# Optimization experiments

Hardware: AMD Instinct MI355X
Metric: run time of the kernel (lower is better)

The kernel has to match this reference:

```python
import jax, jax.numpy as jnp
import numpy as np
from jax import lax

H = 512; MEL = 80; B = 8; S = 128; T = 200; NCH = 256


def _lstm_layer(x, Wih, Whh, bih, bhh, reverse=False):
    # x: [B, S, Din] -> [B, S, H]; PyTorch gate order i,f,g,o
    xs = jnp.swapaxes(x, 0, 1)
    bsz = x.shape[0]
    hid = Whh.shape[1]

    def step(carry, xt):
        h, c = carry
        g = xt @ Wih.T + bih + h @ Whh.T + bhh
        i, f, gg, o = jnp.split(g, 4, axis=-1)
        c2 = jax.nn.sigmoid(f) * c + jax.nn.sigmoid(i) * jnp.tanh(gg)
        h2 = jax.nn.sigmoid(o) * jnp.tanh(c2)
        return (h2, c2), h2

    init = (jnp.zeros((bsz, hid), x.dtype), jnp.zeros((bsz, hid), x.dtype))
    _, hs = lax.scan(step, init, xs, reverse=reverse)
    return jnp.swapaxes(hs, 0, 1)


def _forward(text_sequence, target_mel_len, emb, Wih00, Whh00, bih00, bhh00,
             Wih01, Whh01, bih01, bhh01, Wih10, Whh10, bih10, bhh10,
             Wih11, Whh11, bih11, bhh11, attn_W, attn_b, attn_v,
             dec_Wih, dec_Whh, dec_bih, dec_bhh, mel_W, mel_b):
    x = emb[text_sequence]  # [B,S,H] (dropout disabled: eval mode)
    f0 = _lstm_layer(x, Wih00, Whh00, bih00, bhh00)
    b0 = _lstm_layer(x, Wih01, Whh01, bih01, bhh01, reverse=True)
    x1 = jnp.concatenate([f0, b0], axis=-1)
    f1 = _lstm_layer(x1, Wih10, Whh10, bih10, bhh10)
    b1 = _lstm_layer(x1, Wih11, Whh11, bih11, bhh11, reverse=True)
    enc = jnp.concatenate([f1, b1], axis=-1)  # [B,S,2H]

    # attn Linear on cat(hidden, encoder): split weight into hidden/encoder parts
    W_h = attn_W[:, :H]
    W_e = attn_W[:, H:]
    enc_part = jnp.einsum('bsd,hd->bsh', enc, W_e) + attn_b  # hoisted out of loop
    bsz = text_sequence.shape[0]

    def step(carry, _):
        h, c, din = carry
        energy = jnp.tanh(enc_part + (h @ W_h.T)[:, None, :])  # [B,S,H]
        score = energy @ attn_v                                # [B,S]
        a = jax.nn.softmax(score, axis=1)
        ctx = jnp.einsum('bs,bsd->bd', a, enc)                 # [B,2H]
        xin = jnp.concatenate([din, ctx], axis=1)              # [B,MEL+2H]
        g = xin @ dec_Wih.T + dec_bih + h @ dec_Whh.T + dec_bhh
        i, f, gg, o = jnp.split(g, 4, axis=-1)
        c2 = jax.nn.sigmoid(f) * c + jax.nn.sigmoid(i) * jnp.tanh(gg)
        h2 = jax.nn.sigmoid(o) * jnp.tanh(c2)
        mel = h2 @ mel_W.T + mel_b                             # [B,MEL]
        return (h2, c2, mel), mel

    carry0 = (jnp.zeros((bsz, H), jnp.float32),
              jnp.zeros((bsz, H), jnp.float32),
              jnp.zeros((bsz, MEL), jnp.float32))
    _, mels = lax.scan(step, carry0, None, length=target_mel_len)
    return jnp.transpose(mels, (1, 2, 0))  # [B, MEL, T]


def setup_inputs() -> dict:
    key = jax.random.key(0)
    keys = jax.random.split(key, 64)
    ki = iter(range(64))

    def rn(shape, scale=0.05):
        return jax.random.normal(keys[next(ki)], shape, dtype=jnp.float32) * scale

    inp = {}
    inp['text_sequence'] = jax.random.randint(keys[next(ki)], (B, S), 0, NCH)
    inp['target_mel_len'] = T
    inp['emb'] = rn((NCH, H), 0.3)
    for l, din in ((0, H), (1, 2 * H)):
        for d in (0, 1):
            inp[f'Wih{l}{d}'] = rn((4 * H, din))
            inp[f'Whh{l}{d}'] = rn((4 * H, H))
            inp[f'bih{l}{d}'] = rn((4 * H,))
            inp[f'bhh{l}{d}'] = rn((4 * H,))
    inp['attn_W'] = rn((H, 3 * H))
    inp['attn_b'] = rn((H,))
    inp['attn_v'] = rn((H,))
    inp['dec_Wih'] = rn((4 * H, 2 * H + MEL))
    inp['dec_Whh'] = rn((4 * H, H))
    inp['dec_bih'] = rn((4 * H,))
    inp['dec_bhh'] = rn((4 * H,))
    inp['mel_W'] = rn((MEL, H))
    inp['mel_b'] = rn((MEL,))
    return inp


def reference(text_sequence, target_mel_len, emb, Wih00, Whh00, bih00, bhh00,
              Wih01, Whh01, bih01, bhh01, Wih10, Whh10, bih10, bhh10,
              Wih11, Whh11, bih11, bhh11, attn_W, attn_b, attn_v,
              dec_Wih, dec_Whh, dec_bih, dec_bhh, mel_W, mel_b):
    return _forward(text_sequence, target_mel_len, emb, Wih00, Whh00, bih00, bhh00,
                    Wih01, Whh01, bih01, bhh01, Wih10, Whh10, bih10, bhh10,
                    Wih11, Whh11, bih11, bhh11, attn_W, attn_b, attn_v,
                    dec_Wih, dec_Whh, dec_bih, dec_bhh, mel_W, mel_b)
```

## Files before the change

kernel.cpp:

```cpp
#include <hip/hip_runtime.h>

#define B_ 8
#define S_ 128
#define H_ 512
#define G_ 2048
#define MEL_ 80

#define FLG_DEC    0
#define FLG_L0     8192
#define FLG_L1     10240
#define OFF_H0S    12288
#define OFF_H1S    28672
#define OFF_DH     45056
#define OFF_ATT    53248
#define OFF_HW     54272
#define ZERO_WORDS 58368
#define OFF_X0     58368
#define OFF_GX0F   (OFF_X0 + 524288)
#define OFF_GX0B   (OFF_GX0F + 2097152)
#define OFF_H0     (OFF_GX0B + 2097152)
#define OFF_GX1F   (OFF_H0 + 1048576)
#define OFF_GX1B   (OFF_GX1F + 2097152)
#define OFF_ENC    (OFF_GX1B + 2097152)
#define OFF_ENCP   (OFF_ENC + 1048576)
#define OFF_WE     OFF_GX0F
#define OFF_WH2    OFF_GX0B
#define OFF_BA     (OFF_GX0B + 1048576)
#define OFF_BB     (OFF_GX0B + 1050624)

__device__ __forceinline__ float sigm_f(float x) {
    x = fminf(fmaxf(x, -30.f), 30.f);
    return 1.f / (1.f + __expf(-x));
}
__device__ __forceinline__ float tanh_f(float x) {
    x = fminf(fmaxf(x, -15.f), 15.f);
    float e = __expf(2.f * x);
    return (e - 1.f) / (e + 1.f);
}

__device__ __forceinline__ void agw_u(unsigned* p, unsigned v) {
    __hip_atomic_store(p, v, __ATOMIC_RELAXED, __HIP_MEMORY_SCOPE_AGENT);
}
__device__ __forceinline__ unsigned agr_u(const unsigned* p) {
    return __hip_atomic_load(p, __ATOMIC_RELAXED, __HIP_MEMORY_SCOPE_AGENT);
}
__device__ __forceinline__ void agw_f(float* p, float v) {
    agw_u((unsigned*)p, __float_as_uint(v));
}

__device__ __forceinline__ float4 agr_f4(const float* p) {
    float4 v;
    asm volatile("global_load_dwordx4 %0, %1, off sc1\n\t"
                 "s_waitcnt vmcnt(0)"
                 : "=v"(v) : "v"(p) : "memory");
    return v;
}

__global__ __launch_bounds__(256) void zero_kernel(float* p) {
    p[blockIdx.x * 256 + threadIdx.x] = 0.f;
}

__global__ __launch_bounds__(256) void embed_kernel(const int* __restrict__ text,
                                                    const float* __restrict__ emb,
                                                    float* __restrict__ X) {
    int i = blockIdx.x * 256 + threadIdx.x;
    int bs = i >> 7;
    int h4 = i & 127;
    int ch = text[bs];
    ((float4*)X)[i] = ((const float4*)emb)[ch * 128 + h4];
}

__global__ __launch_bounds__(256) void gemm_f32(const float* __restrict__ A, int lda,
                                                const float* __restrict__ W, int ldw,
                                                const float* __restrict__ b1,
                                                const float* __restrict__ b2,
                                                float* __restrict__ C, int ldc, int K) {
    __shared__ float As[32][68];
    __shared__ float Ws[32][68];
    int tid = threadIdx.x;
    int tx = tid & 15, ty = tid >> 4;
    int n0 = blockIdx.x * 64, m0 = blockIdx.y * 64;
    float acc[4][4] = {};
    int r  = tid >> 3;
    int c4 = (tid & 7) * 4;
    for (int k0 = 0; k0 < K; k0 += 32) {
        float4 a0 = *(const float4*)&A[(m0 + r) * lda + k0 + c4];
        float4 a1 = *(const float4*)&A[(m0 + r + 32) * lda + k0 + c4];
        float4 w0 = *(const float4*)&W[(n0 + r) * ldw + k0 + c4];
        float4 w1 = *(const float4*)&W[(n0 + r + 32) * ldw + k0 + c4];
        As[c4 + 0][r] = a0.x; As[c4 + 1][r] = a0.y; As[c4 + 2][r] = a0.z; As[c4 + 3][r] = a0.w;
        As[c4 + 0][r + 32] = a1.x; As[c4 + 1][r + 32] = a1.y; As[c4 + 2][r + 32] = a1.z; As[c4 + 3][r + 32] = a1.w;
        Ws[c4 + 0][r] = w0.x; Ws[c4 + 1][r] = w0.y; Ws[c4 + 2][r] = w0.z; Ws[c4 + 3][r] = w0.w;
        Ws[c4 + 0][r + 32] = w1.x; Ws[c4 + 1][r + 32] = w1.y; Ws[c4 + 2][r + 32] = w1.z; Ws[c4 + 3][r + 32] = w1.w;
        __syncthreads();
#pragma unroll 8
        for (int kk = 0; kk < 32; ++kk) {
            float4 av = *(const float4*)&As[kk][ty * 4];
            float4 wv = *(const float4*)&Ws[kk][tx * 4];
            acc[0][0] = fmaf(av.x, wv.x, acc[0][0]); acc[0][1] = fmaf(av.x, wv.y, acc[0][1]);
            acc[0][2] = fmaf(av.x, wv.z, acc[0][2]); acc[0][3] = fmaf(av.x, wv.w, acc[0][3]);
            acc[1][0] = fmaf(av.y, wv.x, acc[1][0]); acc[1][1] = fmaf(av.y, wv.y, acc[1][1]);
            acc[1][2] = fmaf(av.y, wv.z, acc[1][2]); acc[1][3] = fmaf(av.y, wv.w, acc[1][3]);
            acc[2][0] = fmaf(av.z, wv.x, acc[2][0]); acc[2][1] = fmaf(av.z, wv.y, acc[2][1]);
            acc[2][2] = fmaf(av.z, wv.z, acc[2][2]); acc[2][3] = fmaf(av.z, wv.w, acc[2][3]);
            acc[3][0] = fmaf(av.w, wv.x, acc[3][0]); acc[3][1] = fmaf(av.w, wv.y, acc[3][1]);
            acc[3][2] = fmaf(av.w, wv.z, acc[3][2]); acc[3][3] = fmaf(av.w, wv.w, acc[3][3]);
        }
        __syncthreads();
    }
#pragma unroll
    for (int i = 0; i < 4; ++i)
#pragma unroll
        for (int j = 0; j < 4; ++j) {
            int n = n0 + tx * 4 + j;
            int m = m0 + ty * 4 + i;
            float bias = (b1 ? b1[n] : 0.f) + (b2 ? b2[n] : 0.f);
            C[m * ldc + n] = acc[i][j] + bias;
        }
}

__global__ __launch_bounds__(256) void we_kernel(const float* __restrict__ Wih,
                                                 const float* __restrict__ ENC,
                                                 float* __restrict__ WE) {
    const float* A = Wih + 80;
    const float* W = ENC + (size_t)blockIdx.z * 131072;
    float* C = WE + (size_t)blockIdx.z * 262144;
    __shared__ float As[32][68];
    __shared__ float Ws[32][68];
    int tid = threadIdx.x;
    int tx = tid & 15, ty = tid >> 4;
    int n0 = blockIdx.x * 64, m0 = blockIdx.y * 64;
    float acc[4][4] = {};
    int r  = tid >> 3;
    int c4 = (tid & 7) * 4;
    for (int k0 = 0; k0 < 1024; k0 += 32) {
        float4 a0 = *(const float4*)&A[(size_t)(m0 + r) * 1104 + k0 + c4];
        float4 a1 = *(const float4*)&A[(size_t)(m0 + r + 32) * 1104 + k0 + c4];
        float4 w0 = *(const float4*)&W[(n0 + r) * 1024 + k0 + c4];
        float4 w1 = *(const float4*)&W[(n0 + r + 32) * 1024 + k0 + c4];
        As[c4 + 0][r] = a0.x; As[c4 + 1][r] = a0.y; As[c4 + 2][r] = a0.z; As[c4 + 3][r] = a0.w;
        As[c4 + 0][r + 32] = a1.x; As[c4 + 1][r + 32] = a1.y; As[c4 + 2][r + 32] = a1.z; As[c4 + 3][r + 32] = a1.w;
        Ws[c4 + 0][r] = w0.x; Ws[c4 + 1][r] = w0.y; Ws[c4 + 2][r] = w0.z; Ws[c4 + 3][r] = w0.w;
        Ws[c4 + 0][r + 32] = w1.x; Ws[c4 + 1][r + 32] = w1.y; Ws[c4 + 2][r + 32] = w1.z; Ws[c4 + 3][r + 32] = w1.w;
        __syncthreads();
#pragma unroll 8
        for (int kk = 0; kk < 32; ++kk) {
            float4 av = *(const float4*)&As[kk][ty * 4];
            float4 wv = *(const float4*)&Ws[kk][tx * 4];
            acc[0][0] = fmaf(av.x, wv.x, acc[0][0]); acc[0][1] = fmaf(av.x, wv.y, acc[0][1]);
            acc[0][2] = fmaf(av.x, wv.z, acc[0][2]); acc[0][3] = fmaf(av.x, wv.w, acc[0][3]);
            acc[1][0] = fmaf(av.y, wv.x, acc[1][0]); acc[1][1] = fmaf(av.y, wv.y, acc[1][1]);
            acc[1][2] = fmaf(av.y, wv.z, acc[1][2]); acc[1][3] = fmaf(av.y, wv.w, acc[1][3]);
            acc[2][0] = fmaf(av.z, wv.x, acc[2][0]); acc[2][1] = fmaf(av.z, wv.y, acc[2][1]);
            acc[2][2] = fmaf(av.z, wv.z, acc[2][2]); acc[2][3] = fmaf(av.z, wv.w, acc[2][3]);
            acc[3][0] = fmaf(av.w, wv.x, acc[3][0]); acc[3][1] = fmaf(av.w, wv.y, acc[3][1]);
            acc[3][2] = fmaf(av.w, wv.z, acc[3][2]); acc[3][3] = fmaf(av.w, wv.w, acc[3][3]);
        }
        __syncthreads();
    }
#pragma unroll
    for (int i = 0; i < 4; ++i)
#pragma unroll
        for (int j = 0; j < 4; ++j)
            C[(size_t)(m0 + ty * 4 + i) * 128 + n0 + tx * 4 + j] = acc[i][j];
}

__global__ __launch_bounds__(256) void wh2_kernel(const float* __restrict__ Wih,
                                                  const float* __restrict__ Whh,
                                                  const float* __restrict__ melW,
                                                  float* __restrict__ WH2) {
    int wg = blockIdx.x;
    int tid = threadIdx.x;
    int r = wg >> 1;
    int k = (wg & 1) * 256 + tid;
    __shared__ float wrow[80];
    if (tid < 80) wrow[tid] = Wih[(size_t)r * 1104 + tid];
    __syncthreads();
    float acc = Whh[(size_t)r * 512 + k];
#pragma unroll 8
    for (int m = 0; m < 80; ++m)
        acc = fmaf(wrow[m], melW[m * 512 + k], acc);
    WH2[(size_t)r * 512 + k] = acc;
}

__global__ __launch_bounds__(256) void bias_kernel(const float* __restrict__ Wih,
                                                   const float* __restrict__ bih,
                                                   const float* __restrict__ bhh,
                                                   const float* __restrict__ melb,
                                                   float* __restrict__ BA,
                                                   float* __restrict__ BB) {
    int r = blockIdx.x * 256 + threadIdx.x;
    float a = bih[r] + bhh[r];
    float b2 = 0.f;
#pragma unroll 8
    for (int m = 0; m < 80; ++m)
        b2 = fmaf(Wih[(size_t)r * 1104 + m], melb[m], b2);
    BA[r] = a;
    BB[r] = a + b2;
}

__global__ __launch_bounds__(256) void lstm_kernel(const float* __restrict__ GXf,
                                                   const float* __restrict__ GXb,
                                                   const float* __restrict__ Whh_f,
                                                   const float* __restrict__ Whh_b,
                                                   float* __restrict__ Hout,
                                                   float* __restrict__ hstate,
                                                   unsigned* __restrict__ flagsL) {
    int wg  = blockIdx.x;
    int s   = wg & 7;
    int g16 = wg >> 3;
    int dir = g16 >> 3;
    int b   = g16 & 7;
    const float* GX  = dir ? GXb : GXf;
    const float* Whh = dir ? Whh_b : Whh_f;
    float* hs = hstate + g16 * 1024;
    unsigned* fg = flagsL + g16 * 128;

    int tid = threadIdx.x;
    int g = tid >> 6, c = tid & 63;
    int grow = g * 512 + s * 64 + c;
    const float* wr = Whh + (size_t)grow * 512;

    __shared__ float hsh[512];
    __shared__ float gvL[4][64];

    float cst = 0.f;

    for (int t = 0; t < 128; ++t) {
        if (tid < 128) {
            const unsigned* f = fg + (tid >> 4) * 16;
            while (agr_u(f) < (unsigned)t)
                __builtin_amdgcn_s_sleep(1);
            *(float4*)&hsh[tid * 4] = agr_f4(hs + (t & 1) * 512 + tid * 4);
        }
        __syncthreads();

        int st = dir ? (127 - t) : t;
        float acc = GX[((size_t)b * S_ + st) * G_ + grow];
        float a0 = 0.f, a1 = 0.f, a2 = 0.f, a3 = 0.f;
#pragma unroll 8
        for (int k = 0; k < 512; k += 4) {
            float4 wv = *(const float4*)(wr + k);
            float4 hv = *(const float4*)&hsh[k];
            a0 = fmaf(wv.x, hv.x, a0); a1 = fmaf(wv.y, hv.y, a1);
            a2 = fmaf(wv.z, hv.z, a2); a3 = fmaf(wv.w, hv.w, a3);
        }
        gvL[g][c] = acc + (a0 + a1) + (a2 + a3);
        __syncthreads();

        if (tid < 64) {
            float gi = gvL[0][tid], gf = gvL[1][tid];
            float gg = gvL[2][tid], go = gvL[3][tid];
            float c2 = sigm_f(gf) * cst + sigm_f(gi) * tanh_f(gg);
            float h2 = sigm_f(go) * tanh_f(c2);
            cst = c2;
            agw_f(hs + ((t & 1) ^ 1) * 512 + s * 64 + tid, h2);
            asm volatile("s_waitcnt vmcnt(0)" ::: "memory");
            if (tid == 0)
                agw_u(fg + s * 16, (unsigned)(t + 1));
            Hout[((size_t)b * S_ + st) * 1024 + dir * 512 + s * 64 + tid] = h2;
        }
    }
}

__global__ __launch_bounds__(256) void decoder_kernel(float* __restrict__ ws,
                                                      const float* __restrict__ attn_W,
                                                      const float* __restrict__ attn_v,
                                                      const float* __restrict__ mel_W,
                                                      const float* __restrict__ mel_b,
                                                      float* __restrict__ out, int T,
                                                      unsigned* __restrict__ flags) {
    float* ENCP = ws + OFF_ENCP;
    float* DH   = ws + OFF_DH;
    float* ATT  = ws + OFF_ATT;
    float* HW   = ws + OFF_HW;
    const float* WE  = ws + OFF_WE;
    const float* WH2 = ws + OFF_WH2;
    const float* BA  = ws + OFF_BA;
    const float* BB  = ws + OFF_BB;

    int wg  = blockIdx.x;
    int tid = threadIdx.x;

    if (wg < 128) {
        int s = wg & 15;
        int b = wg >> 4;
        unsigned* fC = flags + b * 1024;
        unsigned* fA = fC + 16 * 16;
        unsigned* fB = fC + 32 * 16;

        int r   = tid >> 1;
        int half = tid & 1;
        int grow = (r >> 5) * 512 + s * 32 + (r & 31);
        const float* wh2_half = WH2 + (size_t)grow * 512 + half * 256;
        const float* we_row   = WE + ((size_t)b * 2048 + grow) * 128 + half * 64;
        float bias_a = (half == 0) ? BA[grow] : 0.f;
        float bias_b = (half == 0) ? BB[grow] : 0.f;
        int r2 = tid & 31, oct = tid >> 5;
        const float* wh_row = attn_W + (size_t)(s * 32 + r2) * 1536 + oct * 64;

        __shared__ float hsh[512];
        __shared__ float hwred[32][9];
        __shared__ float gBx[128][2];
        __shared__ float gv[128];
        __shared__ float attL[128];

        float cst = 0.f;

        for (int t = 0; t < T; ++t) {
            if (tid < 128) {
                const unsigned* f = fC + (tid >> 3) * 16;
                while (agr_u(f) < (unsigned)t)
                    __builtin_amdgcn_s_sleep(1);
                *(float4*)&hsh[tid * 4] = agr_f4(DH + (t & 1) * 4096 + b * 512 + tid * 4);
            }
            __syncthreads();

            {
                const float* hp = hsh + oct * 64;
                float w = 0.f;
#pragma unroll 8
                for (int k = 0; k < 64; k += 4) {
                    float4 wv = *(const float4*)(wh_row + k);
                    float4 hv = *(const float4*)(hp + k);
                    w = fmaf(wv.x, hv.x, w); w = fmaf(wv.y, hv.y, w);
                    w = fmaf(wv.z, hv.z, w); w = fmaf(wv.w, hv.w, w);
                }
                hwred[r2][oct] = w;
            }
            __syncthreads();
            if (tid < 32) {
                float hw = hwred[tid][0] + hwred[tid][1] + hwred[tid][2] + hwred[tid][3]
                         + hwred[tid][4] + hwred[tid][5] + hwred[tid][6] + hwred[tid][7];
                agw_f(HW + b * 512 + s * 32 + tid, hw);
                asm volatile("s_waitcnt vmcnt(0)" ::: "memory");
                if (tid == 0)
                    agw_u(fA + s * 16, (unsigned)(t + 1));
            }

            float wpart = (t == 0) ? bias_a : bias_b;
            {
                const float* hp = hsh + half * 256;
                float a0 = 0.f, a1 = 0.f, a2 = 0.f, a3 = 0.f;
#pragma unroll 8
                for (int k = 0; k < 256; k += 4) {
                    float4 wv = *(const float4*)(wh2_half + k);
                    float4 hv = *(const float4*)(hp + k);
                    a0 = fmaf(wv.x, hv.x, a0); a1 = fmaf(wv.y, hv.y, a1);
                    a2 = fmaf(wv.z, hv.z, a2); a3 = fmaf(wv.w, hv.w, a3);
                }
                wpart += (a0 + a1) + (a2 + a3);
            }

            if (tid < 32) {
                while (agr_u(fB) < (unsigned)(t + 1))
                    __builtin_amdgcn_s_sleep(1);
                *(float4*)&attL[tid * 4] = agr_f4(ATT + b * 128 + tid * 4);
            }
            __syncthreads();

            {
                const float* ap = attL + half * 64;
                float a0 = 0.f, a1 = 0.f, a2 = 0.f, a3 = 0.f;
#pragma unroll 8
                for (int k = 0; k < 64; k += 4) {
                    float4 wv = *(const float4*)(we_row + k);
                    a0 = fmaf(wv.x, ap[k + 0], a0); a1 = fmaf(wv.y, ap[k + 1], a1);
                    a2 = fmaf(wv.z, ap[k + 2], a2); a3 = fmaf(wv.w, ap[k + 3], a3);
                }
                gBx[r][half] = wpart + (a0 + a1) + (a2 + a3);
            }
            __syncthreads();
            if (tid < 128)
                gv[tid] = gBx[tid][0] + gBx[tid][1];
            __syncthreads();
            if (tid < 32) {
                float gi = gv[tid], gf = gv[32 + tid], gg = gv[64 + tid], go = gv[96 + tid];
                float c2 = sigm_f(gf) * cst + sigm_f(gi) * tanh_f(gg);
                float h2 = sigm_f(go) * tanh_f(c2);
                cst = c2;
                agw_f(DH + ((t + 1) & 1) * 4096 + b * 512 + s * 32 + tid, h2);
                asm volatile("s_waitcnt vmcnt(0)" ::: "memory");
                if (tid == 0)
                    agw_u(fC + s * 16, (unsigned)(t + 1));
            }
        }
    } else {
        int b = wg - 128;
        unsigned* fC = flags + b * 1024;
        unsigned* fA = fC + 16 * 16;
        unsigned* fB = fC + 32 * 16;

        __shared__ float hw2[512];
        __shared__ float dh2[512];
        __shared__ float scred[128][2];
        __shared__ float red[128];
        __shared__ float att[128];
        __shared__ float melp[80][2];

        int r = tid >> 1, half = tid & 1;

        for (int t = 0; t < T; ++t) {
            if (tid < 128) {
                const unsigned* f = fA + (tid >> 3) * 16;
                while (agr_u(f) < (unsigned)(t + 1))
                    __builtin_amdgcn_s_sleep(1);
                *(float4*)&hw2[tid * 4] = agr_f4(HW + b * 512 + tid * 4);
            }
            __syncthreads();

            {
                int sI = tid & 127, kh = tid >> 7;
                const float* ep = ENCP + ((size_t)b * S_ + sI) * 512 + kh * 256;
                const float* hp = hw2 + kh * 256;
                const float* vv = attn_v + kh * 256;
                float a0 = 0.f, a1 = 0.f, a2 = 0.f, a3 = 0.f;
#pragma unroll 4
                for (int k = 0; k < 256; k += 4) {
                    float4 e4 = *(const float4*)(ep + k);
                    float4 h4 = *(const float4*)(hp + k);
                    float4 v4 = *(const float4*)(vv + k);
                    a0 = fmaf(tanh_f(e4.x + h4.x), v4.x, a0);
                    a1 = fmaf(tanh_f(e4.y + h4.y), v4.y, a1);
                    a2 = fmaf(tanh_f(e4.z + h4.z), v4.z, a2);
                    a3 = fmaf(tanh_f(e4.w + h4.w), v4.w, a3);
                }
                scred[sI][kh] = (a0 + a1) + (a2 + a3);
            }
            __syncthreads();

            float sc = 0.f;
            if (tid < 128) {
                sc = scred[tid][0] + scred[tid][1];
                red[tid] = sc;
            }
            __syncthreads();
            for (int off = 64; off >= 1; off >>= 1) {
                if (tid < off) red[tid] = fmaxf(red[tid], red[tid + off]);
                __syncthreads();
            }
            float mx = red[0];
            __syncthreads();
            if (tid < 128) {
                float e = __expf(sc - mx);
                att[tid] = e;
                red[tid] = e;
            }
            __syncthreads();
            if (tid < 64) red[tid] += red[tid + 64];
            __syncthreads();
            for (int off = 32; off >= 1; off >>= 1) {
                if (tid < off) red[tid] += red[tid + off];
                __syncthreads();
            }
            float inv = 1.f / red[0];

            if (tid < 32) {
                agw_f(ATT + b * 128 + tid * 4 + 0, att[tid * 4 + 0] * inv);
                agw_f(ATT + b * 128 + tid * 4 + 1, att[tid * 4 + 1] * inv);
                agw_f(ATT + b * 128 + tid * 4 + 2, att[tid * 4 + 2] * inv);
                agw_f(ATT + b * 128 + tid * 4 + 3, att[tid * 4 + 3] * inv);
                asm volatile("s_waitcnt vmcnt(0)" ::: "memory");
                if (tid == 0)
                    agw_u(fB, (unsigned)(t + 1));
            }

            if (t > 0) {
                if (tid < 128) {
                    const unsigned* f = fC + (tid >> 3) * 16;
                    while (agr_u(f) < (unsigned)t)
                        __builtin_amdgcn_s_sleep(1);
                    *(float4*)&dh2[tid * 4] = agr_f4(DH + (t & 1) * 4096 + b * 512 + tid * 4);
                }
                __syncthreads();
                if (tid < 160) {
                    const float* wp = mel_W + (size_t)r * 512 + half * 256;
                    const float* hp = dh2 + half * 256;
                    float a0 = 0.f, a1 = 0.f, a2 = 0.f, a3 = 0.f;
#pragma unroll 8
                    for (int k = 0; k < 256; k += 4) {
                        float4 wv = *(const float4*)(wp + k);
                        float4 hv = *(const float4*)(hp + k);
                        a0 = fmaf(wv.x, hv.x, a0); a1 = fmaf(wv.y, hv.y, a1);
                        a2 = fmaf(wv.z, hv.z, a2); a3 = fmaf(wv.w, hv.w, a3);
                    }
                    melp[r][half] = (a0 + a1) + (a2 + a3);
                }
                __syncthreads();
                if (tid < 80)
                    out[b * MEL_ * T + tid * T + (t - 1)] = melp[tid][0] + melp[tid][1] + mel_b[tid];
            }
        }

        if (tid < 128) {
            const unsigned* f = fC + (tid >> 3) * 16;
            while (agr_u(f) < (unsigned)T)
                __builtin_amdgcn_s_sleep(1);
            *(float4*)&dh2[tid * 4] = agr_f4(DH + (T & 1) * 4096 + b * 512 + tid * 4);
        }
        __syncthreads();
        if (tid < 160) {
            const float* wp = mel_W + (size_t)r * 512 + half * 256;
            const float* hp = dh2 + half * 256;
            float a0 = 0.f, a1 = 0.f, a2 = 0.f, a3 = 0.f;
#pragma unroll 8
            for (int k = 0; k < 256; k += 4) {
                float4 wv = *(const float4*)(wp + k);
                float4 hv = *(const float4*)(hp + k);
                a0 = fmaf(wv.x, hv.x, a0); a1 = fmaf(wv.y, hv.y, a1);
                a2 = fmaf(wv.z, hv.z, a2); a3 = fmaf(wv.w, hv.w, a3);
            }
            melp[r][half] = (a0 + a1) + (a2 + a3);
        }
        __syncthreads();
        if (tid < 80)
            out[b * MEL_ * T + tid * T + (T - 1)] = melp[tid][0] + melp[tid][1] + mel_b[tid];
    }
}

extern "C" void kernel_launch(void* const* d_in, const int* in_sizes, int n_in,
                              void* d_out, int out_size, void* d_ws, size_t ws_size,
                              hipStream_t stream) {
    const int*   text  = (const int*)d_in[0];
    const float* emb   = (const float*)d_in[2];
    const float* Wih00 = (const float*)d_in[3];
    const float* Whh00 = (const float*)d_in[4];
    const float* bih00 = (const float*)d_in[5];
    const float* bhh00 = (const float*)d_in[6];
    const float* Wih01 = (const float*)d_in[7];
    const float* Whh01 = (const float*)d_in[8];
    const float* bih01 = (const float*)d_in[9];
    const float* bhh01 = (const float*)d_in[10];
    const float* Wih10 = (const float*)d_in[11];
    const float* Whh10 = (const float*)d_in[12];
    const float* bih10 = (const float*)d_in[13];
    const float* bhh10 = (const float*)d_in[14];
    const float* Wih11 = (const float*)d_in[15];
    const float* Whh11 = (const float*)d_in[16];
    const float* bih11 = (const float*)d_in[17];
    const float* bhh11 = (const float*)d_in[18];
    const float* attn_W = (const float*)d_in[19];
    const float* attn_b = (const float*)d_in[20];
    const float* attn_v = (const float*)d_in[21];
    const float* dec_Wih = (const float*)d_in[22];
    const float* dec_Whh = (const float*)d_in[23];
    const float* dec_bih = (const float*)d_in[24];
    const float* dec_bhh = (const float*)d_in[25];
    const float* mel_W = (const float*)d_in[26];
    const float* mel_b = (const float*)d_in[27];

    float* ws = (float*)d_ws;
    unsigned* flags = (unsigned*)d_ws;
    float* out = (float*)d_out;
    int T = out_size / (B_ * MEL_);

    zero_kernel<<<ZERO_WORDS / 256, 256, 0, stream>>>(ws);

    embed_kernel<<<512, 256, 0, stream>>>(text, emb, ws + OFF_X0);

    gemm_f32<<<dim3(32, 16), 256, 0, stream>>>(ws + OFF_X0, 512, Wih00, 512,
                                               bih00, bhh00, ws + OFF_GX0F, 2048, 512);
    gemm_f32<<<dim3(32, 16), 256, 0, stream>>>(ws + OFF_X0, 512, Wih01, 512,
                                               bih01, bhh01, ws + OFF_GX0B, 2048, 512);
    lstm_kernel<<<128, 256, 0, stream>>>(ws + OFF_GX0F, ws + OFF_GX0B, Whh00, Whh01,
                                         ws + OFF_H0, ws + OFF_H0S, flags + FLG_L0);
    wh2_kernel<<<4096, 256, 0, stream>>>(dec_Wih, dec_Whh, mel_W, ws + OFF_WH2);
    bias_kernel<<<8, 256, 0, stream>>>(dec_Wih, dec_bih, dec_bhh, mel_b,
                                       ws + OFF_BA, ws + OFF_BB);
    gemm_f32<<<dim3(32, 16), 256, 0, stream>>>(ws + OFF_H0, 1024, Wih10, 1024,
                                               bih10, bhh10, ws + OFF_GX1F, 2048, 1024);
    gemm_f32<<<dim3(32, 16), 256, 0, stream>>>(ws + OFF_H0, 1024, Wih11, 1024,
                                               bih11, bhh11, ws + OFF_GX1B, 2048, 1024);
    lstm_kernel<<<128, 256, 0, stream>>>(ws + OFF_GX1F, ws + OFF_GX1B, Whh10, Whh11,
                                         ws + OFF_ENC, ws + OFF_H1S, flags + FLG_L1);
    gemm_f32<<<dim3(8, 16), 256, 0, stream>>>(ws + OFF_ENC, 1024, attn_W + 512, 1536,
                                              attn_b, nullptr, ws + OFF_ENCP, 512, 1024);
    we_kernel<<<dim3(2, 32, 8), 256, 0, stream>>>(dec_Wih, ws + OFF_ENC, ws + OFF_WE);
    decoder_kernel<<<136, 256, 0, stream>>>(ws, attn_W, attn_v, mel_W, mel_b, out, T,
                                            flags + FLG_DEC);
}
```

Baseline: 9.927 ms.

## Compute attention hidden projection as partial sums after cell update to shorten critical path

The h·W_h attention projection is no longer computed at the start of each decoder step by the cell workgroups. Instead, each cell workgroup multiplies its freshly computed 32-element slice of h2 against the matching columns of attn_W and publishes 512-wide partial sums. The attention workgroup waits on a new per-slice flag and reduces the 16 partials itself. This takes the projection off the step's serial critical path and removes one cross-workgroup handshake, at the cost of more global traffic for the partial sums plus an extra zeroing launch.

Result: no change. 9.902 ms (-0.3%).

```diff
diff --git a/kernel.cpp b/kernel.cpp
--- a/kernel.cpp
+++ b/kernel.cpp
@@ -27,6 +27,7 @@
 #define OFF_WH2    OFF_GX0B
 #define OFF_BA     (OFF_GX0B + 1048576)
 #define OFF_BB     (OFF_GX0B + 1050624)
+#define OFF_HWP    OFF_GX1F
 
 __device__ __forceinline__ float sigm_f(float x) {
     x = fminf(fmaxf(x, -30.f), 30.f);
@@ -54,6 +55,21 @@
                  "s_waitcnt vmcnt(0)"
                  : "=v"(v) : "v"(p) : "memory");
     return v;
+}
+__device__ __forceinline__ void agw_f4(float* p, float4 v) {
+    agw_f(p + 0, v.x); agw_f(p + 1, v.y); agw_f(p + 2, v.z); agw_f(p + 3, v.w);
+    asm volatile("s_waitcnt vmcnt(0)" ::: "memory");
+}
+__device__ __forceinline__ void agr_f4x4(const float* p0, const float* p1,
+                                         const float* p2, const float* p3,
+                                         float4& a, float4& b, float4& c, float4& d) {
+    asm volatile("global_load_dwordx4 %0, %4, off sc1\n\t"
+                 "global_load_dwordx4 %1, %5, off sc1\n\t"
+                 "global_load_dwordx4 %2, %6, off sc1\n\t"
+                 "global_load_dwordx4 %3, %7, off sc1\n\t"
+                 "s_waitcnt vmcnt(0)"
+                 : "=&v"(a), "=&v"(b), "=&v"(c), "=&v"(d)
+                 : "v"(p0), "v"(p1), "v"(p2), "v"(p3) : "memory");
 }
 
 __global__ __launch_bounds__(256) void zero_kernel(float* p) {
@@ -273,7 +289,7 @@
     float* ENCP = ws + OFF_ENCP;
     float* DH   = ws + OFF_DH;
     float* ATT  = ws + OFF_ATT;
-    float* HW   = ws + OFF_HW;
+    float* HWP  = ws + OFF_HWP;
     const float* WE  = ws + OFF_WE;
     const float* WH2 = ws + OFF_WH2;
     const float* BA  = ws + OFF_BA;
@@ -285,9 +301,9 @@
     if (wg < 128) {
         int s = wg & 15;
         int b = wg >> 4;
-        unsigned* fC = flags + b * 1024;
-        unsigned* fA = fC + 16 * 16;
-        unsigned* fB = fC + 32 * 16;
+        unsigned* fCh = flags + b * 1024;
+        unsigned* fCp = fCh + 256;
+        unsigned* fB  = fCh + 512;
 
         int r   = tid >> 1;
         int half = tid & 1;
@@ -296,47 +312,23 @@
         const float* we_row   = WE + ((size_t)b * 2048 + grow) * 128 + half * 64;
         float bias_a = (half == 0) ? BA[grow] : 0.f;
         float bias_b = (half == 0) ? BB[grow] : 0.f;
-        int r2 = tid & 31, oct = tid >> 5;
-        const float* wh_row = attn_W + (size_t)(s * 32 + r2) * 1536 + oct * 64;
 
         __shared__ float hsh[512];
-        __shared__ float hwred[32][9];
         __shared__ float gBx[128][2];
         __shared__ float gv[128];
         __shared__ float attL[128];
+        __shared__ float h2sh[32];
 
         float cst = 0.f;
 
         for (int t = 0; t < T; ++t) {
             if (tid < 128) {
-                const unsigned* f = fC + (tid >> 3) * 16;
+                const unsigned* f = fCh + (tid >> 3) * 16;
                 while (agr_u(f) < (unsigned)t)
                     __builtin_amdgcn_s_sleep(1);
                 *(float4*)&hsh[tid * 4] = agr_f4(DH + (t & 1) * 4096 + b * 512 + tid * 4);
             }
             __syncthreads();
-
-            {
-                const float* hp = hsh + oct * 64;
-                float w = 0.f;
-#pragma unroll 8
-                for (int k = 0; k < 64; k += 4) {
-                    float4 wv = *(const float4*)(wh_row + k);
-                    float4 hv = *(const float4*)(hp + k);
-                    w = fmaf(wv.x, hv.x, w); w = fmaf(wv.y, hv.y, w);
-                    w = fmaf(wv.z, hv.z, w); w = fmaf(wv.w, hv.w, w);
-                }
-                hwred[r2][oct] = w;
-            }
-            __syncthreads();
-            if (tid < 32) {
-                float hw = hwred[tid][0] + hwred[tid][1] + hwred[tid][2] + hwred[tid][3]
-                         + hwred[tid][4] + hwred[tid][5] + hwred[tid][6] + hwred[tid][7];
-                agw_f(HW + b * 512 + s * 32 + tid, hw);
-                asm volatile("s_waitcnt vmcnt(0)" ::: "memory");
-                if (tid == 0)
-                    agw_u(fA + s * 16, (unsigned)(t + 1));
-            }
 
             float wpart = (t == 0) ? bias_a : bias_b;
             {
@@ -374,23 +366,49 @@
             if (tid < 128)
                 gv[tid] = gBx[tid][0] + gBx[tid][1];
             __syncthreads();
+
             if (tid < 32) {
                 float gi = gv[tid], gf = gv[32 + tid], gg = gv[64 + tid], go = gv[96 + tid];
                 float c2 = sigm_f(gf) * cst + sigm_f(gi) * tanh_f(gg);
                 float h2 = sigm_f(go) * tanh_f(c2);
                 cst = c2;
+                h2sh[tid] = h2;
                 agw_f(DH + ((t + 1) & 1) * 4096 + b * 512 + s * 32 + tid, h2);
                 asm volatile("s_waitcnt vmcnt(0)" ::: "memory");
                 if (tid == 0)
-                    agw_u(fC + s * 16, (unsigned)(t + 1));
-            }
+                    agw_u(fCh + s * 16, (unsigned)(t + 1));
+            }
+            __syncthreads();
+
+            if (tid < 128) {
+                int r0 = tid * 4;
+                float p[4];
+#pragma unroll
+                for (int i = 0; i < 4; ++i) {
+                    const float* wrow2 = attn_W + (size_t)(r0 + i) * 1536 + s * 32;
+                    float a0 = 0.f, a1 = 0.f, a2 = 0.f, a3 = 0.f;
+#pragma unroll
+                    for (int c = 0; c < 32; c += 4) {
+                        float4 wv = *(const float4*)(wrow2 + c);
+                        a0 = fmaf(wv.x, h2sh[c + 0], a0); a1 = fmaf(wv.y, h2sh[c + 1], a1);
+                        a2 = fmaf(wv.z, h2sh[c + 2], a2); a3 = fmaf(wv.w, h2sh[c + 3], a3);
+                    }
+                    p[i] = (a0 + a1) + (a2 + a3);
+                }
+                float4 v; v.x = p[0]; v.y = p[1]; v.z = p[2]; v.w = p[3];
+                agw_f4(HWP + ((size_t)(b * 16 + s)) * 512 + r0, v);
+            }
+            __syncthreads();
+            if (tid == 0)
+                agw_u(fCp + s * 16, (unsigned)(t + 1));
         }
     } else {
         int b = wg - 128;
-        unsigned* fC = flags + b * 1024;
-        unsigned* fA = fC + 16 * 16;
-        unsigned* fB = fC + 32 * 16;
-
+        unsigned* fCh = flags + b * 1024;
+        unsigned* fCp = fCh + 256;
+        unsigned* fB  = fCh + 512;
+
+        __shared__ float hwp2[2][512];
         __shared__ float hw2[512];
         __shared__ float dh2[512];
         __shared__ float scred[128][2];
@@ -401,11 +419,33 @@
         int r = tid >> 1, half = tid & 1;
 
         for (int t = 0; t < T; ++t) {
+            if (tid < 16) {
+                while (agr_u(fCp + tid * 16) < (unsigned)t)
+                    __builtin_amdgcn_s_sleep(1);
+            }
+            __syncthreads();
+
+            {
+                int c4 = (tid & 127), jh = tid >> 7;
+                const float* base = HWP + (size_t)b * 8192 + (size_t)jh * 8 * 512 + c4 * 4;
+                float4 v0, v1, v2, v3, v4, v5, v6, v7;
+                agr_f4x4(base + 0 * 512, base + 1 * 512, base + 2 * 512, base + 3 * 512,
+                         v0, v1, v2, v3);
+                agr_f4x4(base + 4 * 512, base + 5 * 512, base + 6 * 512, base + 7 * 512,
+                         v4, v5, v6, v7);
+                float4 sum;
+                sum.x = ((v0.x + v1.x) + (v2.x + v3.x)) + ((v4.x + v5.x) + (v6.x + v7.x));
+                sum.y = ((v0.y + v1.y) + (v2.y + v3.y)) + ((v4.y + v5.y) + (v6.y + v7.y));
+                sum.z = ((v0.z + v1.z) + (v2.z + v3.z)) + ((v4.z + v5.z) + (v6.z + v7.z));
+                sum.w = ((v0.w + v1.w) + (v2.w + v3.w)) + ((v4.w + v5.w) + (v6.w + v7.w));
+                *(float4*)&hwp2[jh][c4 * 4] = sum;
+            }
+            __syncthreads();
             if (tid < 128) {
-                const unsigned* f = fA + (tid >> 3) * 16;
-                while (agr_u(f) < (unsigned)(t + 1))
-                    __builtin_amdgcn_s_sleep(1);
-                *(float4*)&hw2[tid * 4] = agr_f4(HW + b * 512 + tid * 4);
+                float4 a = *(const float4*)&hwp2[0][tid * 4];
+                float4 c = *(const float4*)&hwp2[1][tid * 4];
+                float4 s4; s4.x = a.x + c.x; s4.y = a.y + c.y; s4.z = a.z + c.z; s4.w = a.w + c.w;
+                *(float4*)&hw2[tid * 4] = s4;
             }
             __syncthreads();
 
@@ -466,12 +506,8 @@
             }
 
             if (t > 0) {
-                if (tid < 128) {
-                    const unsigned* f = fC + (tid >> 3) * 16;
-                    while (agr_u(f) < (unsigned)t)
-                        __builtin_amdgcn_s_sleep(1);
+                if (tid < 128)
                     *(float4*)&dh2[tid * 4] = agr_f4(DH + (t & 1) * 4096 + b * 512 + tid * 4);
-                }
                 __syncthreads();
                 if (tid < 160) {
                     const float* wp = mel_W + (size_t)r * 512 + half * 256;
@@ -489,15 +525,18 @@
                 __syncthreads();
                 if (tid < 80)
                     out[b * MEL_ * T + tid * T + (t - 1)] = melp[tid][0] + melp[tid][1] + mel_b[tid];
-            }
-        }
-
-        if (tid < 128) {
-            const unsigned* f = fC + (tid >> 3) * 16;
-            while (agr_u(f) < (unsigned)T)
+            } else {
+                __syncthreads();
+            }
+        }
+
+        if (tid < 16) {
+            while (agr_u(fCh + tid * 16) < (unsigned)T)
                 __builtin_amdgcn_s_sleep(1);
+        }
+        __syncthreads();
+        if (tid < 128)
             *(float4*)&dh2[tid * 4] = agr_f4(DH + (T & 1) * 4096 + b * 512 + tid * 4);
-        }
         __syncthreads();
         if (tid < 160) {
             const float* wp = mel_W + (size_t)r * 512 + half * 256;
@@ -576,6 +615,7 @@
     gemm_f32<<<dim3(8, 16), 256, 0, stream>>>(ws + OFF_ENC, 1024, attn_W + 512, 1536,
                                               attn_b, nullptr, ws + OFF_ENCP, 512, 1024);
     we_kernel<<<dim3(2, 32, 8), 256, 0, stream>>>(dec_Wih, ws + OFF_ENC, ws + OFF_WE);
+    zero_kernel<<<65536 / 256, 256, 0, stream>>>(ws + OFF_HWP);
     decoder_kernel<<<136, 256, 0, stream>>>(ws, attn_W, attn_v, mel_W, mel_b, out, T,
                                             flags + FLG_DEC);
 }
```
